# Kernel tuning notes

Hardware: AMD Instinct MI355X
Metric: run time of the kernel (lower is better)

Reference implementation:

```python
import jax, jax.numpy as jnp
import numpy as np

N_NODES = 40000
EMB = 256
NHEADS = 2
HEAD = EMB // NHEADS
NLAYERS = 4
NGNN = 2
LN_EPS = 1e-5
LEAKY = 0.01


def setup_inputs() -> dict:
    key = jax.random.key(0)
    ks = iter(jax.random.split(key, 40))
    nrm = lambda shape, s=0.05: jax.random.normal(next(ks), shape, dtype=jnp.float32) * s
    inp = {
        'feat0': nrm((20000, 512), 1.0),
        'feat1': nrm((20000, 512), 1.0),
        'fc_w0': nrm((256, 512)), 'fc_b0': jnp.zeros((256,), jnp.float32),
        'fc_w1': nrm((256, 512)), 'fc_b1': jnp.zeros((256,), jnp.float32),
        'gcn_w': nrm((NGNN, 256, 256)),
        'edge_src': jax.random.randint(next(ks), (640000,), 0, N_NODES),
        'edge_dst': jax.random.randint(next(ks), (640000,), 0, N_NODES),
        'dg_seqs': jax.random.randint(next(ks), (1024, 64), 0, N_NODES),
        'pt_seqs': jax.random.randint(next(ks), (1024, 64), 0, N_NODES),
        'type_emb': nrm((4, 4), 1.0),
        'node_type': jax.random.randint(next(ks), (N_NODES,), 0, 4),
        'gt_wl': nrm((8, 256, 256)), 'gt_wr': nrm((8, 256, 256)),
        'gt_al': nrm((8, 1, HEAD)), 'gt_ar': nrm((8, 1, HEAD)),
        'gt_wf': nrm((8, 256, 256)),
        'ln_g': jnp.ones((8, 256), jnp.float32), 'ln_b': jnp.zeros((8, 256), jnp.float32),
        'proj_d_w': nrm((2, 256, 256)), 'proj_d_b': jnp.zeros((2, 256), jnp.float32),
        'proj_p_w': nrm((2, 256, 256)), 'proj_p_b': jnp.zeros((2, 256), jnp.float32),
        'ml_w1': nrm((256, 512)), 'ml_b1': jnp.zeros((256,), jnp.float32),
        'ml_w2': nrm((128, 256)), 'ml_b2': jnp.zeros((128,), jnp.float32),
        'ml_w3': nrm((1, 128)), 'ml_b3': jnp.zeros((1,), jnp.float32),
    }
    return inp


def _layernorm(x, g, b):
    m = x.mean(-1, keepdims=True)
    v = ((x - m) ** 2).mean(-1, keepdims=True)
    return (x - m) * jax.lax.rsqrt(v + LN_EPS) * g + b


def _leaky(x):
    return jnp.where(x >= 0, x, LEAKY * x)


def _agt_layer(h, wl, wr, al, ar, wf, g, b):
    # h: [B, L, EMB]; additive (GAT-style) attention, temper = 1.0
    B, L, _ = h.shape
    fl = (h @ wl.T).reshape(B, L, NHEADS, HEAD).transpose(0, 2, 1, 3)  # [B,H,L,hd]
    fr = (h @ wr.T).reshape(B, L, NHEADS, HEAD).transpose(0, 2, 1, 3)
    sl = _leaky(fl) @ al.T                     # [B,H,L,1]
    sr = _leaky(fr) @ ar.T                     # [B,H,L,1]
    score = jax.nn.softmax(sl + sr.transpose(0, 1, 3, 2), axis=-1)  # [B,H,L,L]
    ctx = score @ fr                           # [B,H,L,hd]
    h_sa = ctx.transpose(0, 2, 1, 3).reshape(B, L, EMB)
    return _layernorm(h + h_sa @ wf.T, g, b)


def _gcn(gh, W, src, dst):
    # DGL GraphConv norm='both', allow_zero_in_degree, activation=relu
    ones = jnp.ones(src.shape[0], gh.dtype)
    deg_out = jnp.clip(jax.ops.segment_sum(ones, src, num_segments=N_NODES), 1.0)
    deg_in = jnp.clip(jax.ops.segment_sum(ones, dst, num_segments=N_NODES), 1.0)
    x = gh * (deg_out ** -0.5)[:, None]
    x = x @ W
    agg = jax.ops.segment_sum(x[src], dst, num_segments=N_NODES)
    return jax.nn.relu(agg * (deg_in ** -0.5)[:, None])


def reference(feat0, feat1, fc_w0, fc_b0, fc_w1, fc_b1, gcn_w, edge_src, edge_dst,
              dg_seqs, pt_seqs, type_emb, node_type, gt_wl, gt_wr, gt_al, gt_ar,
              gt_wf, ln_g, ln_b, proj_d_w, proj_d_b, proj_p_w, proj_p_b,
              ml_w1, ml_b1, ml_w2, ml_b2, ml_w3, ml_b3):
    # per-type input projections, concatenated along node dim
    h0 = feat0 @ fc_w0.T + fc_b0
    h1 = feat1 @ fc_w1.T + fc_b1
    gh = jnp.concatenate([h0, h1], axis=0)  # [N, EMB]
    r = type_emb[node_type]                 # computed but unused downstream (faithful)
    for layer in range(NGNN):
        gh = _gcn(gh, gcn_w[layer], edge_src, edge_dst)
    # graph transformer per node type (dropout = identity in eval)
    embs = []
    for t, seqs in ((0, dg_seqs), (1, pt_seqs)):
        h = gh[seqs]                        # [B, L, EMB]
        _ = r[seqs]
        for l in range(NLAYERS):
            i = t * NLAYERS + l
            h = _agt_layer(h, gt_wl[i], gt_wr[i], gt_al[i], gt_ar[i], gt_wf[i], ln_g[i], ln_b[i])
        embs.append(h[:, 0, :])
    dg_emb, pt_emb = embs
    # Proj heads: linear -> elu -> linear
    dg_emb = jax.nn.elu(dg_emb @ proj_d_w[0].T + proj_d_b[0]) @ proj_d_w[1].T + proj_d_b[1]
    pt_emb = jax.nn.elu(pt_emb @ proj_p_w[0].T + proj_p_b[0]) @ proj_p_w[1].T + proj_p_b[1]
    # Predict MLP on concat
    x = jnp.concatenate([dg_emb, pt_emb], axis=1)  # [B, 512]
    x = jax.nn.relu(x @ ml_w1.T + ml_b1)
    x = jax.nn.relu(x @ ml_w2.T + ml_b2)
    out = jax.nn.sigmoid(x @ ml_w3.T + ml_b3)
    return out.reshape(x.shape[0])
```

## Files before the change

kernel.cpp:

```cpp
#include <hip/hip_runtime.h>
#include <hip/hip_bf16.h>
#include <math.h>

typedef unsigned int u32;
typedef unsigned short u16;
typedef __attribute__((ext_vector_type(8))) short bf16x8;
typedef __attribute__((ext_vector_type(4))) float f32x4;

__device__ __forceinline__ float b2f(u16 u) { union { u32 i; float f; } c; c.i = ((u32)u) << 16; return c.f; }
__device__ __forceinline__ u16 f2b(float f) { __hip_bfloat16 h = __float2bfloat16(f); u16 r; __builtin_memcpy(&r, &h, 2); return r; }
__device__ __forceinline__ float b2f_lo(u32 w) { union { u32 i; float f; } c; c.i = w << 16; return c.f; }
__device__ __forceinline__ float b2f_hi(u32 w) { union { u32 i; float f; } c; c.i = w & 0xffff0000u; return c.f; }
__device__ __forceinline__ u32 pk2(float a, float b) { return (u32)f2b(a) | ((u32)f2b(b) << 16); }

__device__ __forceinline__ float wave_sum(float v) {
    #pragma unroll
    for (int off = 32; off > 0; off >>= 1) v += __shfl_xor(v, off, 64);
    return v;
}
__device__ __forceinline__ float wave_max(float v) {
    #pragma unroll
    for (int off = 32; off > 0; off >>= 1) v = fmaxf(v, __shfl_xor(v, off, 64));
    return v;
}

template<bool AF32>
__global__ __launch_bounds__(256) void mfma_gemm_kernel(
    const void* __restrict__ Av, const u16* __restrict__ B,
    const float* __restrict__ bias, const float* __restrict__ rowscale,
    u16* __restrict__ Cb, int M, int N, int K,
    const void* __restrict__ Av1, const u16* __restrict__ B1,
    const float* __restrict__ bias1, u16* __restrict__ Cb1)
{
    if (blockIdx.z) { Av = Av1; B = B1; bias = bias1; Cb = Cb1; }
    __shared__ u16 lds[(64 + 128) * 64];
    const int tid = threadIdx.x;
    const int wid = tid >> 6, lane = tid & 63;
    const int wr = wid >> 1, wc = wid & 1;
    const int m0 = blockIdx.y * 64, n0 = blockIdx.x * 128;

    f32x4 acc[2][4] = {};

    for (int k0 = 0; k0 < K; k0 += 64) {
        #pragma unroll
        for (int s = 0; s < 2; ++s) {
            int idx = tid + s * 256;
            int row = idx >> 3, g = idx & 7;
            int row_g = m0 + row; if (row_g >= M) row_g = M - 1;
            int swz = ((g << 4) ^ ((row & 7) << 4));
            if (AF32) {
                const float* src = (const float*)Av + (size_t)row_g * K + k0 + g * 8;
                float4 v0 = *(const float4*)src;
                float4 v1 = *(const float4*)(src + 4);
                uint4 pk;
                pk.x = pk2(v0.x, v0.y); pk.y = pk2(v0.z, v0.w);
                pk.z = pk2(v1.x, v1.y); pk.w = pk2(v1.z, v1.w);
                *(uint4*)((char*)lds + row * 128 + swz) = pk;
            } else {
                f32x4 v = *(const f32x4*)((const u16*)Av + (size_t)row_g * K + k0 + g * 8);
                *(f32x4*)((char*)lds + row * 128 + swz) = v;
            }
        }
        #pragma unroll
        for (int s = 0; s < 4; ++s) {
            int idx = tid + s * 256;
            int row = idx >> 3, g = idx & 7;
            int row_g = n0 + row; if (row_g >= N) row_g = N - 1;
            f32x4 v = *(const f32x4*)(B + (size_t)row_g * K + k0 + g * 8);
            *(f32x4*)((char*)lds + 8192 + row * 128 + ((g << 4) ^ ((row & 7) << 4))) = v;
        }
        __syncthreads();
        #pragma unroll
        for (int ks = 0; ks < 2; ++ks) {
            const int off = (ks * 64 + ((lane >> 4) << 4)) ^ ((lane & 7) << 4);
            const int ra = lane & 15;
            bf16x8 af[2], bfr[4];
            #pragma unroll
            for (int i = 0; i < 2; ++i)
                af[i] = *(bf16x8*)((char*)lds + (wr * 32 + i * 16 + ra) * 128 + off);
            #pragma unroll
            for (int j = 0; j < 4; ++j)
                bfr[j] = *(bf16x8*)((char*)lds + 8192 + (wc * 64 + j * 16 + ra) * 128 + off);
            #pragma unroll
            for (int i = 0; i < 2; ++i)
                #pragma unroll
                for (int j = 0; j < 4; ++j)
                    acc[i][j] = __builtin_amdgcn_mfma_f32_16x16x32_bf16(af[i], bfr[j], acc[i][j], 0, 0, 0);
        }
        __syncthreads();
    }

    const int cr = lane >> 4, ccol = lane & 15;
    #pragma unroll
    for (int i = 0; i < 2; ++i) {
        #pragma unroll
        for (int j = 0; j < 4; ++j) {
            int colg = n0 + wc * 64 + j * 16 + ccol;
            if (colg >= N) continue;
            float badd = bias ? bias[colg] : 0.f;
            #pragma unroll
            for (int reg = 0; reg < 4; ++reg) {
                int rowg = m0 + wr * 32 + i * 16 + cr * 4 + reg;
                if (rowg >= M) continue;
                float v = acc[i][j][reg] + badd;
                if (rowscale) v *= rowscale[rowg];
                Cb[(size_t)rowg * N + colg] = f2b(v);
            }
        }
    }
}

__global__ __launch_bounds__(512, 4) void fused_transformer_kernel(
    const float* __restrict__ gh, const int* __restrict__ dg_seqs,
    const int* __restrict__ pt_seqs,
    const u16* __restrict__ wrN,
    const u32* __restrict__ wfT2,
    const float* __restrict__ ar,
    const float* __restrict__ lng, const float* __restrict__ lnb,
    float* __restrict__ embT)
{
    __shared__ u16 ldsA[64 * 256];
    float* sPartO = (float*)ldsA;
    float* pbufO  = sPartO + 512;
    float* ctxO   = pbufO + 128;
    float* uO     = ctxO + 256;

    const int tid = threadIdx.x;
    const int bx = blockIdx.x;
    const int t = bx >> 10, s = bx & 1023;
    const int r = tid >> 3, o8 = tid & 7;
    const int wid = tid >> 6, lane = tid & 63;
    const int hd = wid >> 2;
    const int g4 = lane >> 4, cl = lane & 15;

    const int* seqs = t ? pt_seqs : dg_seqs;

    float4 y[8];
    {
        int node = seqs[s * 64 + r];
        const float* src = gh + (size_t)node * 256 + o8 * 32;
        #pragma unroll
        for (int v = 0; v < 8; ++v) y[v] = *(const float4*)(src + v * 4);
    }

    for (int l = 0; l < 4; ++l) {
        const int li = t * 4 + l;
        {
            const int c = o8 >> 1, gb = (o8 & 1) * 4;
            #pragma unroll
            for (int gg = 0; gg < 4; ++gg) {
                float4 a = y[2 * gg], b = y[2 * gg + 1];
                uint4 pk;
                pk.x = pk2(a.x, a.y); pk.y = pk2(a.z, a.w);
                pk.z = pk2(b.x, b.y); pk.w = pk2(b.z, b.w);
                int g = gb + gg;
                *(uint4*)((char*)ldsA + c * 8192 + r * 128 + ((g << 4) ^ ((r & 7) << 4))) = pk;
            }
        }
        __syncthreads();

        f32x4 acc[4][2] = {};
        {
            const u16* wrl = wrN + (size_t)li * 65536;
            const int ra = lane & 15;
            #pragma unroll
            for (int kc = 0; kc < 8; ++kc) {
                const int c = kc >> 1, ks = kc & 1;
                const int off = (ks * 64 + ((lane >> 4) << 4)) ^ ((lane & 7) << 4);
                bf16x8 af[4], bfr[2];
                #pragma unroll
                for (int i = 0; i < 4; ++i)
                    af[i] = *(bf16x8*)((char*)ldsA + c * 8192 + (i * 16 + ra) * 128 + off);
                #pragma unroll
                for (int j = 0; j < 2; ++j)
                    bfr[j] = *(const bf16x8*)(wrl + ((size_t)((wid * 2 + j) * 8 + kc) << 9) + lane * 8);
                #pragma unroll
                for (int i = 0; i < 4; ++i)
                    #pragma unroll
                    for (int j = 0; j < 2; ++j)
                        acc[i][j] = __builtin_amdgcn_mfma_f32_16x16x32_bf16(af[i], bfr[j], acc[i][j], 0, 0, 0);
            }
        }
        __syncthreads();

        {
            const float* arl = ar + li * 128;
            float arj[2];
            #pragma unroll
            for (int j = 0; j < 2; ++j) arj[j] = arl[(wid & 3) * 32 + j * 16 + cl];
            #pragma unroll
            for (int i = 0; i < 4; ++i)
                #pragma unroll
                for (int reg = 0; reg < 4; ++reg) {
                    float sc;
                    {
                        float x0 = acc[i][0][reg], x1 = acc[i][1][reg];
                        sc = (x0 >= 0.f ? x0 : 0.01f * x0) * arj[0]
                           + (x1 >= 0.f ? x1 : 0.01f * x1) * arj[1];
                    }
                    sc += __shfl_xor(sc, 1, 64);
                    sc += __shfl_xor(sc, 2, 64);
                    sc += __shfl_xor(sc, 4, 64);
                    sc += __shfl_xor(sc, 8, 64);
                    if (cl == 0) sPartO[wid * 64 + i * 16 + g4 * 4 + reg] = sc;
                }
        }
        __syncthreads();

        {
            int base = hd * 4 * 64;
            float sv = sPartO[base + lane] + sPartO[base + 64 + lane]
                     + sPartO[base + 128 + lane] + sPartO[base + 192 + lane];
            float mx = wave_max(sv);
            float e = expf(sv - mx);
            float sm = wave_sum(e);
            if ((wid & 3) == 0) pbufO[hd * 64 + lane] = e / sm;
        }
        __syncthreads();

        {
            float pv[4][4];
            #pragma unroll
            for (int i = 0; i < 4; ++i)
                #pragma unroll
                for (int reg = 0; reg < 4; ++reg)
                    pv[i][reg] = pbufO[hd * 64 + i * 16 + g4 * 4 + reg];
            #pragma unroll
            for (int j = 0; j < 2; ++j) {
                float c = 0.f;
                #pragma unroll
                for (int i = 0; i < 4; ++i)
                    #pragma unroll
                    for (int reg = 0; reg < 4; ++reg)
                        c = fmaf(pv[i][reg], acc[i][j][reg], c);
                c += __shfl_xor(c, 16, 64);
                c += __shfl_xor(c, 32, 64);
                if (g4 == 0) ctxO[wid * 32 + j * 16 + cl] = c;
            }
        }
        __syncthreads();

        {
            const int n = tid & 255, half = tid >> 8;
            const u32* wp = wfT2 + (size_t)li * 32768 + (size_t)half * 16384 + n;
            const float* cx = ctxO + half * 128;
            float ua0 = 0.f, ua1 = 0.f, ua2 = 0.f, ua3 = 0.f;
            #pragma unroll 4
            for (int d2 = 0; d2 < 64; d2 += 4) {
                u32 w0 = wp[(size_t)(d2 + 0) * 256];
                u32 w1 = wp[(size_t)(d2 + 1) * 256];
                u32 w2 = wp[(size_t)(d2 + 2) * 256];
                u32 w3 = wp[(size_t)(d2 + 3) * 256];
                ua0 = fmaf(cx[2 * d2 + 0], b2f_lo(w0), ua0);
                ua0 = fmaf(cx[2 * d2 + 1], b2f_hi(w0), ua0);
                ua1 = fmaf(cx[2 * d2 + 2], b2f_lo(w1), ua1);
                ua1 = fmaf(cx[2 * d2 + 3], b2f_hi(w1), ua1);
                ua2 = fmaf(cx[2 * d2 + 4], b2f_lo(w2), ua2);
                ua2 = fmaf(cx[2 * d2 + 5], b2f_hi(w2), ua2);
                ua3 = fmaf(cx[2 * d2 + 6], b2f_lo(w3), ua3);
                ua3 = fmaf(cx[2 * d2 + 7], b2f_hi(w3), ua3);
            }
            uO[half * 256 + n] = (ua0 + ua1) + (ua2 + ua3);
        }
        __syncthreads();

        {
            #pragma unroll
            for (int v = 0; v < 8; ++v) {
                int c0 = o8 * 32 + v * 4;
                float4 u0 = *(const float4*)&uO[c0];
                float4 u1 = *(const float4*)&uO[256 + c0];
                y[v].x += u0.x + u1.x; y[v].y += u0.y + u1.y;
                y[v].z += u0.z + u1.z; y[v].w += u0.w + u1.w;
            }
            float sm = 0.f, qq = 0.f;
            #pragma unroll
            for (int v = 0; v < 8; ++v) {
                sm += y[v].x + y[v].y + y[v].z + y[v].w;
                qq += y[v].x * y[v].x + y[v].y * y[v].y + y[v].z * y[v].z + y[v].w * y[v].w;
            }
            sm += __shfl_xor(sm, 1, 64); sm += __shfl_xor(sm, 2, 64); sm += __shfl_xor(sm, 4, 64);
            qq += __shfl_xor(qq, 1, 64); qq += __shfl_xor(qq, 2, 64); qq += __shfl_xor(qq, 4, 64);
            float mean = sm * (1.f / 256.f);
            float var = qq * (1.f / 256.f) - mean * mean;
            float inv = rsqrtf(var + 1e-5f);
            const float* gl = lng + li * 256 + o8 * 32;
            const float* bl = lnb + li * 256 + o8 * 32;
            if (l < 3) {
                #pragma unroll
                for (int v = 0; v < 8; ++v) {
                    float4 gv = *(const float4*)(gl + v * 4);
                    float4 bv = *(const float4*)(bl + v * 4);
                    y[v].x = (y[v].x - mean) * inv * gv.x + bv.x;
                    y[v].y = (y[v].y - mean) * inv * gv.y + bv.y;
                    y[v].z = (y[v].z - mean) * inv * gv.z + bv.z;
                    y[v].w = (y[v].w - mean) * inv * gv.w + bv.w;
                }
            } else if (r == 0) {
                float* dst = embT + (size_t)(t * 1024 + s) * 256 + o8 * 32;
                #pragma unroll
                for (int v = 0; v < 8; ++v) {
                    float4 gv = *(const float4*)(gl + v * 4);
                    float4 bv = *(const float4*)(bl + v * 4);
                    float4 o;
                    o.x = (y[v].x - mean) * inv * gv.x + bv.x;
                    o.y = (y[v].y - mean) * inv * gv.y + bv.y;
                    o.z = (y[v].z - mean) * inv * gv.z + bv.z;
                    o.w = (y[v].w - mean) * inv * gv.w + bv.w;
                    *(float4*)(dst + v * 4) = o;
                }
            }
        }
        __syncthreads();
    }
}

template<bool BT>
__global__ __launch_bounds__(256) void gemm_kernel(
    const float* __restrict__ A, const float* __restrict__ B,
    const float* __restrict__ bias, const float* __restrict__ rowscale,
    float* __restrict__ C,
    int M, int N, int K, int lda, int ldb, int ldc, int coff, int act,
    const float* __restrict__ A1, const float* __restrict__ B1,
    const float* __restrict__ bias1, float* __restrict__ C1, int coff1)
{
    if (blockIdx.z) { A = A1; B = B1; bias = bias1; C = C1; coff = coff1; }
    __shared__ float As[32][64 + 4];
    __shared__ float Bs[32][64 + 4];
    const int tid = threadIdx.x;
    const int m0 = blockIdx.y * 64;
    const int n0 = blockIdx.x * 64;
    const int ty = tid >> 4, tx = tid & 15;
    float acc[4][4] = {};
    for (int k0 = 0; k0 < K; k0 += 32) {
        #pragma unroll
        for (int r = 0; r < 2; ++r) {
            int f4 = tid + r * 256;
            int arw = f4 >> 3, af = (f4 & 7) << 2;
            float4 v = make_float4(0.f, 0.f, 0.f, 0.f);
            int grow = m0 + arw;
            if (grow < M) {
                v = *(const float4*)(A + (size_t)grow * lda + k0 + af);
                if (rowscale) { float s = rowscale[grow]; v.x *= s; v.y *= s; v.z *= s; v.w *= s; }
            }
            As[af + 0][arw] = v.x; As[af + 1][arw] = v.y; As[af + 2][arw] = v.z; As[af + 3][arw] = v.w;
        }
        #pragma unroll
        for (int r = 0; r < 2; ++r) {
            int f4 = tid + r * 256;
            int col = f4 >> 3, kf = (f4 & 7) << 2;
            float4 v = make_float4(0.f, 0.f, 0.f, 0.f);
            if (n0 + col < N) v = *(const float4*)(B + (size_t)(n0 + col) * ldb + k0 + kf);
            Bs[kf + 0][col] = v.x; Bs[kf + 1][col] = v.y; Bs[kf + 2][col] = v.z; Bs[kf + 3][col] = v.w;
        }
        __syncthreads();
        #pragma unroll
        for (int kk = 0; kk < 32; ++kk) {
            float4 a4 = *(const float4*)&As[kk][ty << 2];
            float4 b4 = *(const float4*)&Bs[kk][tx << 2];
            float a[4] = {a4.x, a4.y, a4.z, a4.w};
            float b[4] = {b4.x, b4.y, b4.z, b4.w};
            #pragma unroll
            for (int i = 0; i < 4; ++i)
                #pragma unroll
                for (int j = 0; j < 4; ++j)
                    acc[i][j] = fmaf(a[i], b[j], acc[i][j]);
        }
        __syncthreads();
    }
    #pragma unroll
    for (int i = 0; i < 4; ++i) {
        int row = m0 + (ty << 2) + i;
        if (row >= M) continue;
        #pragma unroll
        for (int j = 0; j < 4; ++j) {
            int col = n0 + (tx << 2) + j;
            if (col >= N) continue;
            float v = acc[i][j];
            if (bias) v += bias[col];
            if (act == 1) v = fmaxf(v, 0.f);
            else if (act == 2) v = (v > 0.f) ? v : expm1f(v);
            C[(size_t)row * ldc + coff + col] = v;
        }
    }
}

__global__ __launch_bounds__(256) void conv_flat_kernel(const float* __restrict__ in, u16* __restrict__ out, int n) {
    int i = (blockIdx.x * 256 + threadIdx.x) * 4;
    if (i >= n) return;
    float4 v = *(const float4*)(in + i);
    *(uint2*)(out + i) = make_uint2(pk2(v.x, v.y), pk2(v.z, v.w));
}
__global__ __launch_bounds__(256) void conv_gcnw_kernel(const float* __restrict__ w, u16* __restrict__ out) {
    int idx = blockIdx.x * 256 + threadIdx.x;
    int l = blockIdx.y;
    int k = idx >> 8, n = idx & 255;
    out[(size_t)l * 65536 + n * 256 + k] = f2b(w[(size_t)l * 65536 + k * 256 + n]);
}
__global__ __launch_bounds__(256) void conv_wrN_kernel(const float* __restrict__ w, u16* __restrict__ out) {
    int idx = blockIdx.x * 256 + threadIdx.x;
    int lane = idx & 63;
    int kc = (idx >> 6) & 7;
    int gn = (idx >> 9) & 15;
    int l = idx >> 13;
    int row = gn * 16 + (lane & 15);
    int k0 = kc * 32 + (lane >> 4) * 8;
    const float* src = w + ((size_t)l * 256 + row) * 256 + k0;
    float4 v0 = *(const float4*)src;
    float4 v1 = *(const float4*)(src + 4);
    uint4 pk;
    pk.x = pk2(v0.x, v0.y); pk.y = pk2(v0.z, v0.w);
    pk.z = pk2(v1.x, v1.y); pk.w = pk2(v1.z, v1.w);
    *(uint4*)(out + (size_t)idx * 8) = pk;
}
__global__ __launch_bounds__(256) void conv_wfT2_kernel(const float* __restrict__ w, u32* __restrict__ out) {
    int idx = blockIdx.x * 256 + threadIdx.x;
    int n = idx & 255;
    int d2 = (idx >> 8) & 127;
    int l = idx >> 15;
    const float* src = w + ((size_t)l * 256 + n) * 256 + 2 * d2;
    out[idx] = pk2(src[0], src[1]);
}

#define EDGE_CAP 128
__global__ __launch_bounds__(256) void bucket_fill_kernel(
    const int* __restrict__ src, const int* __restrict__ dst,
    int* __restrict__ ebuf, int* __restrict__ cursor, int* __restrict__ cnt_out, int ne)
{
    int e0 = (blockIdx.x * 256 + threadIdx.x) * 4;
    if (e0 >= ne) return;
    int4 s4 = *(const int4*)(src + e0);
    int4 d4 = *(const int4*)(dst + e0);
    atomicAdd(&cnt_out[s4.x], 1);
    atomicAdd(&cnt_out[s4.y], 1);
    atomicAdd(&cnt_out[s4.z], 1);
    atomicAdd(&cnt_out[s4.w], 1);
    int p0 = atomicAdd(&cursor[d4.x], 1);
    int p1 = atomicAdd(&cursor[d4.y], 1);
    int p2 = atomicAdd(&cursor[d4.z], 1);
    int p3 = atomicAdd(&cursor[d4.w], 1);
    if (p0 < EDGE_CAP) ebuf[(size_t)d4.x * EDGE_CAP + p0] = s4.x;
    if (p1 < EDGE_CAP) ebuf[(size_t)d4.y * EDGE_CAP + p1] = s4.y;
    if (p2 < EDGE_CAP) ebuf[(size_t)d4.z * EDGE_CAP + p2] = s4.z;
    if (p3 < EDGE_CAP) ebuf[(size_t)d4.w * EDGE_CAP + p3] = s4.w;
}
__global__ __launch_bounds__(256) void deg_fin_kernel(const int* __restrict__ cnt, float* __restrict__ dinv, int n) {
    int i = blockIdx.x * 256 + threadIdx.x;
    if (i < n) dinv[i] = rsqrtf(fmaxf((float)cnt[i], 1.0f));
}

__global__ __launch_bounds__(256) void csr_agg_kernel(
    const u16* __restrict__ x, const int* __restrict__ ebuf,
    const int* __restrict__ deg, float* __restrict__ outf, u16* __restrict__ outb, int nnodes)
{
    int n = blockIdx.x * 4 + (threadIdx.x >> 6);
    if (n >= nnodes) return;
    int lane = threadIdx.x & 63;
    int d = deg[n];
    float dinv = rsqrtf(fmaxf((float)d, 1.0f));
    if (d > EDGE_CAP) d = EDGE_CAP;
    const int* eb = ebuf + (size_t)n * EDGE_CAP;
    const int co = lane << 2;
    float a0 = 0.f, a1 = 0.f, a2 = 0.f, a3 = 0.f;
    int k = 0;
    for (; k + 4 <= d; k += 4) {
        int4 s4 = *(const int4*)(eb + k);
        uint2 va = *(const uint2*)(x + (size_t)s4.x * 256 + co);
        uint2 vb = *(const uint2*)(x + (size_t)s4.y * 256 + co);
        uint2 vc = *(const uint2*)(x + (size_t)s4.z * 256 + co);
        uint2 vd = *(const uint2*)(x + (size_t)s4.w * 256 + co);
        a0 += b2f_lo(va.x) + b2f_lo(vb.x) + b2f_lo(vc.x) + b2f_lo(vd.x);
        a1 += b2f_hi(va.x) + b2f_hi(vb.x) + b2f_hi(vc.x) + b2f_hi(vd.x);
        a2 += b2f_lo(va.y) + b2f_lo(vb.y) + b2f_lo(vc.y) + b2f_lo(vd.y);
        a3 += b2f_hi(va.y) + b2f_hi(vb.y) + b2f_hi(vc.y) + b2f_hi(vd.y);
    }
    for (; k < d; ++k) {
        int s = eb[k];
        uint2 v = *(const uint2*)(x + (size_t)s * 256 + co);
        a0 += b2f_lo(v.x); a1 += b2f_hi(v.x);
        a2 += b2f_lo(v.y); a3 += b2f_hi(v.y);
    }
    a0 = fmaxf(a0 * dinv, 0.f); a1 = fmaxf(a1 * dinv, 0.f);
    a2 = fmaxf(a2 * dinv, 0.f); a3 = fmaxf(a3 * dinv, 0.f);
    *(float4*)(outf + (size_t)n * 256 + co) = make_float4(a0, a1, a2, a3);
    *(uint2*)(outb + (size_t)n * 256 + co) = make_uint2(pk2(a0, a1), pk2(a2, a3));
}

__global__ __launch_bounds__(256) void final_kernel(
    const float* __restrict__ m2, const float* __restrict__ w3,
    const float* __restrict__ b3, float* __restrict__ out, int nrows)
{
    int row = blockIdx.x * 4 + (threadIdx.x >> 6);
    int lane = threadIdx.x & 63;
    if (row >= nrows) return;
    float s = m2[(size_t)row * 128 + lane] * w3[lane]
            + m2[(size_t)row * 128 + 64 + lane] * w3[64 + lane];
    s = wave_sum(s);
    if (lane == 0) out[row] = 1.f / (1.f + expf(-(s + b3[0])));
}

static inline int cdiv(int a, int b) { return (a + b - 1) / b; }

extern "C" void kernel_launch(void* const* d_in, const int* in_sizes, int n_in,
                              void* d_out, int out_size, void* d_ws, size_t ws_size,
                              hipStream_t stream)
{
    const float* feat0   = (const float*)d_in[0];
    const float* feat1   = (const float*)d_in[1];
    const float* fc_w0   = (const float*)d_in[2];
    const float* fc_b0   = (const float*)d_in[3];
    const float* fc_w1   = (const float*)d_in[4];
    const float* fc_b1   = (const float*)d_in[5];
    const float* gcn_w   = (const float*)d_in[6];
    const int*   edge_src= (const int*)d_in[7];
    const int*   edge_dst= (const int*)d_in[8];
    const int*   dg_seqs = (const int*)d_in[9];
    const int*   pt_seqs = (const int*)d_in[10];
    const float* gt_wr   = (const float*)d_in[14];
    const float* gt_ar   = (const float*)d_in[16];
    const float* gt_wf   = (const float*)d_in[17];
    const float* ln_g    = (const float*)d_in[18];
    const float* ln_b    = (const float*)d_in[19];
    const float* proj_d_w= (const float*)d_in[20];
    const float* proj_d_b= (const float*)d_in[21];
    const float* proj_p_w= (const float*)d_in[22];
    const float* proj_p_b= (const float*)d_in[23];
    const float* ml_w1   = (const float*)d_in[24];
    const float* ml_b1   = (const float*)d_in[25];
    const float* ml_w2   = (const float*)d_in[26];
    const float* ml_b2   = (const float*)d_in[27];
    const float* ml_w3   = (const float*)d_in[28];
    const float* ml_b3   = (const float*)d_in[29];
    float* out = (float*)d_out;

    float* base  = (float*)d_ws;
    float* gh    = base;
    float* gcnR  = gh + 10240000;
    float* dego  = gcnR + 15440000;
    float* embT  = dego + 40000;
    float* t1    = embT + 524288;
    float* mx    = t1 + 524288;
    float* m1    = mx + 524288;
    float* m2    = m1 + 262144;
    float* wreg  = m2 + 131072;

    u16* tmp_b   = (u16*)gcnR;
    int* ebuf    = (int*)(gcnR + 5120000);
    int* cursor  = ebuf + (size_t)40000 * EDGE_CAP;
    int* cnt_out = cursor + 40000;
    u16* gh_b    = (u16*)(gcnR + 10320000);

    u16* fcw_b   = (u16*)wreg;
    u16* gcnw_b  = fcw_b + 262144;
    u16* wrN     = gcnw_b + 131072;
    u32* wfT2    = (u32*)(wrN + 524288);

    conv_flat_kernel<<<cdiv(131072 / 4, 256), 256, 0, stream>>>(fc_w0, fcw_b, 131072);
    conv_flat_kernel<<<cdiv(131072 / 4, 256), 256, 0, stream>>>(fc_w1, fcw_b + 131072, 131072);
    conv_gcnw_kernel<<<dim3(256, 2), 256, 0, stream>>>(gcn_w, gcnw_b);
    conv_wrN_kernel<<<256, 256, 0, stream>>>(gt_wr, wrN);
    conv_wfT2_kernel<<<1024, 256, 0, stream>>>(gt_wf, wfT2);

    mfma_gemm_kernel<true><<<dim3(2, cdiv(20000, 64), 2), 256, 0, stream>>>(
        feat0, fcw_b, fc_b0, nullptr, gh_b, 20000, 256, 512,
        feat1, fcw_b + 131072, fc_b1, gh_b + (size_t)20000 * 256);

    hipMemsetAsync(cursor, 0, 80000 * sizeof(int), stream);
    bucket_fill_kernel<<<625, 256, 0, stream>>>(edge_src, edge_dst, ebuf, cursor, cnt_out, 640000);
    deg_fin_kernel<<<cdiv(40000, 256), 256, 0, stream>>>(cnt_out, dego, 40000);

    for (int l = 0; l < 2; ++l) {
        mfma_gemm_kernel<false><<<dim3(2, cdiv(40000, 64), 1), 256, 0, stream>>>(
            gh_b, gcnw_b + (size_t)l * 65536, nullptr, dego, tmp_b, 40000, 256, 256,
            gh_b, gcnw_b, nullptr, tmp_b);
        csr_agg_kernel<<<10000, 256, 0, stream>>>(tmp_b, ebuf, cursor, gh, gh_b, 40000);
    }

    fused_transformer_kernel<<<2048, 512, 0, stream>>>(
        gh, dg_seqs, pt_seqs, wrN, wfT2, gt_ar, ln_g, ln_b, embT);

    gemm_kernel<true><<<dim3(4, 16, 2), 256, 0, stream>>>(
        embT, proj_d_w, proj_d_b, nullptr, t1, 1024, 256, 256, 256, 256, 256, 0, 2,
        embT + 262144, proj_p_w, proj_p_b, t1 + 262144, 0);
    gemm_kernel<true><<<dim3(4, 16, 2), 256, 0, stream>>>(
        t1, proj_d_w + 65536, proj_d_b + 256, nullptr, mx, 1024, 256, 256, 256, 256, 512, 0, 0,
        t1 + 262144, proj_p_w + 65536, proj_p_b + 256, mx, 256);

    gemm_kernel<true><<<dim3(4, 16, 1), 256, 0, stream>>>(
        mx, ml_w1, ml_b1, nullptr, m1, 1024, 256, 512, 512, 512, 256, 0, 1,
        mx, ml_w1, ml_b1, m1, 0);
    gemm_kernel<true><<<dim3(2, 16, 1), 256, 0, stream>>>(
        m1, ml_w2, ml_b2, nullptr, m2, 1024, 128, 256, 256, 256, 128, 0, 1,
        m1, ml_w2, ml_b2, m2, 0);
    final_kernel<<<256, 256, 0, stream>>>(m2, ml_w3, ml_b3, out, 1024);
}
```

Measured before the change: 695.5 us.

## Cut barriers in fused transformer by LDS-atomic scores and per-wave softmax

Score partials, context and update buffers get dedicated shared arrays instead of aliasing the MFMA staging tile. That lets the barriers after the MFMA loop and at the end of each layer go away. Per-head scores are now reduced with LDS atomicAdd into a zeroed buffer. Each wave then computes the softmax redundantly in registers, removing the separate softmax barrier and probability buffer. The cost is slightly more LDS per block, extra exp work per wave, and a float summation order that depends on atomic timing.

Measured after the change: 693.4 us. Within noise of the previous version (-0.3%).

```diff
diff --git a/kernel.cpp b/kernel.cpp
--- a/kernel.cpp
+++ b/kernel.cpp
@@ -16,11 +16,6 @@
 __device__ __forceinline__ float wave_sum(float v) {
     #pragma unroll
     for (int off = 32; off > 0; off >>= 1) v += __shfl_xor(v, off, 64);
-    return v;
-}
-__device__ __forceinline__ float wave_max(float v) {
-    #pragma unroll
-    for (int off = 32; off > 0; off >>= 1) v = fmaxf(v, __shfl_xor(v, off, 64));
     return v;
 }
 
@@ -120,10 +115,9 @@
     float* __restrict__ embT)
 {
     __shared__ u16 ldsA[64 * 256];
-    float* sPartO = (float*)ldsA;
-    float* pbufO  = sPartO + 512;
-    float* ctxO   = pbufO + 128;
-    float* uO     = ctxO + 256;
+    __shared__ float scoreH[2][64];
+    __shared__ float ctxS[256];
+    __shared__ float uS[2][256];
 
     const int tid = threadIdx.x;
     const int bx = blockIdx.x;
@@ -156,6 +150,7 @@
                 int g = gb + gg;
                 *(uint4*)((char*)ldsA + c * 8192 + r * 128 + ((g << 4) ^ ((r & 7) << 4))) = pk;
             }
+            if (tid < 128) ((float*)scoreH)[tid] = 0.f;
         }
         __syncthreads();
 
@@ -181,7 +176,6 @@
                         acc[i][j] = __builtin_amdgcn_mfma_f32_16x16x32_bf16(af[i], bfr[j], acc[i][j], 0, 0, 0);
             }
         }
-        __syncthreads();
 
         {
             const float* arl = ar + li * 128;
@@ -202,29 +196,42 @@
                     sc += __shfl_xor(sc, 2, 64);
                     sc += __shfl_xor(sc, 4, 64);
                     sc += __shfl_xor(sc, 8, 64);
-                    if (cl == 0) sPartO[wid * 64 + i * 16 + g4 * 4 + reg] = sc;
+                    if (cl == 0) atomicAdd(&scoreH[hd][i * 16 + g4 * 4 + reg], sc);
                 }
         }
         __syncthreads();
 
+        float p[4][4];
         {
-            int base = hd * 4 * 64;
-            float sv = sPartO[base + lane] + sPartO[base + 64 + lane]
-                     + sPartO[base + 128 + lane] + sPartO[base + 192 + lane];
-            float mx = wave_max(sv);
-            float e = expf(sv - mx);
-            float sm = wave_sum(e);
-            if ((wid & 3) == 0) pbufO[hd * 64 + lane] = e / sm;
-        }
-        __syncthreads();
+            const float* sc = scoreH[hd];
+            #pragma unroll
+            for (int i = 0; i < 4; ++i)
+                *(float4*)p[i] = *(const float4*)(sc + i * 16 + g4 * 4);
+            float mx = -1e30f;
+            #pragma unroll
+            for (int i = 0; i < 4; ++i)
+                #pragma unroll
+                for (int reg = 0; reg < 4; ++reg) mx = fmaxf(mx, p[i][reg]);
+            mx = fmaxf(mx, __shfl_xor(mx, 16, 64));
+            mx = fmaxf(mx, __shfl_xor(mx, 32, 64));
+            float sme = 0.f;
+            #pragma unroll
+            for (int i = 0; i < 4; ++i)
+                #pragma unroll
+                for (int reg = 0; reg < 4; ++reg) {
+                    p[i][reg] = expf(p[i][reg] - mx);
+                    sme += p[i][reg];
+                }
+            sme += __shfl_xor(sme, 16, 64);
+            sme += __shfl_xor(sme, 32, 64);
+            float inv = 1.f / sme;
+            #pragma unroll
+            for (int i = 0; i < 4; ++i)
+                #pragma unroll
+                for (int reg = 0; reg < 4; ++reg) p[i][reg] *= inv;
+        }
 
         {
-            float pv[4][4];
-            #pragma unroll
-            for (int i = 0; i < 4; ++i)
-                #pragma unroll
-                for (int reg = 0; reg < 4; ++reg)
-                    pv[i][reg] = pbufO[hd * 64 + i * 16 + g4 * 4 + reg];
             #pragma unroll
             for (int j = 0; j < 2; ++j) {
                 float c = 0.f;
@@ -232,10 +239,10 @@
                 for (int i = 0; i < 4; ++i)
                     #pragma unroll
                     for (int reg = 0; reg < 4; ++reg)
-                        c = fmaf(pv[i][reg], acc[i][j][reg], c);
+                        c = fmaf(p[i][reg], acc[i][j][reg], c);
                 c += __shfl_xor(c, 16, 64);
                 c += __shfl_xor(c, 32, 64);
-                if (g4 == 0) ctxO[wid * 32 + j * 16 + cl] = c;
+                if (g4 == 0) ctxS[wid * 32 + j * 16 + cl] = c;
             }
         }
         __syncthreads();
@@ -243,7 +250,7 @@
         {
             const int n = tid & 255, half = tid >> 8;
             const u32* wp = wfT2 + (size_t)li * 32768 + (size_t)half * 16384 + n;
-            const float* cx = ctxO + half * 128;
+            const float* cx = ctxS + half * 128;
             float ua0 = 0.f, ua1 = 0.f, ua2 = 0.f, ua3 = 0.f;
             #pragma unroll 4
             for (int d2 = 0; d2 < 64; d2 += 4) {
@@ -260,7 +267,7 @@
                 ua3 = fmaf(cx[2 * d2 + 6], b2f_lo(w3), ua3);
                 ua3 = fmaf(cx[2 * d2 + 7], b2f_hi(w3), ua3);
             }
-            uO[half * 256 + n] = (ua0 + ua1) + (ua2 + ua3);
+            uS[half][n] = (ua0 + ua1) + (ua2 + ua3);
         }
         __syncthreads();
 
@@ -268,8 +275,8 @@
             #pragma unroll
             for (int v = 0; v < 8; ++v) {
                 int c0 = o8 * 32 + v * 4;
-                float4 u0 = *(const float4*)&uO[c0];
-                float4 u1 = *(const float4*)&uO[256 + c0];
+                float4 u0 = *(const float4*)&uS[0][c0];
+                float4 u1 = *(const float4*)&uS[1][c0];
                 y[v].x += u0.x + u1.x; y[v].y += u0.y + u1.y;
                 y[v].z += u0.z + u1.z; y[v].w += u0.w + u1.w;
             }
@@ -311,7 +318,6 @@
                 }
             }
         }
-        __syncthreads();
     }
 }
 
```
